# Performance work log

Measured on AMD Instinct MI355X. Metric: run time of the kernel, lower is better.

The kernel has to match this reference:

```python
import jax, jax.numpy as jnp
import numpy as np
import math

B, C, HLAT, WLON = 1, 256, 46, 90
HEADS = 8
KC = 256   # k_channels (defaults to in_channels)
OC = 256   # out_channels (defaults to in_channels)


def _cc_weights(n):
    # Clenshaw-Curtis quadrature weights on n nodes x_k = cos(k*pi/(n-1)) over [-1, 1]
    # (torch-harmonics 'equiangular' grid quadrature); weights sum to 2.
    N = n - 1
    k = np.arange(n)
    j = np.arange(1, N // 2 + 1)
    b = np.where(2 * j == N, 1.0, 2.0)
    s = (b / (4.0 * j**2 - 1.0))[None, :] * np.cos(2.0 * np.pi * np.outer(k, j) / N)
    w = (1.0 - s.sum(axis=1)) * (2.0 / N)
    w[0] *= 0.5
    w[-1] *= 0.5
    return w


def _log_quad_weights(nlat, nlon):
    wgl = _cc_weights(nlat).astype(np.float32)            # [nlat]
    qw = 2.0 * np.pi * wgl / nlon                          # [nlat]
    qw = np.tile(qw.reshape(-1, 1), (1, nlon)).flatten()   # [nlat*nlon]
    return np.log(qw).reshape(1, 1, -1)                    # (1, 1, N)


def setup_inputs() -> dict:
    key = jax.random.key(0)
    ks = jax.random.split(key, 6)
    scale_qkv = math.sqrt(3.0 / C)
    scale_proj = math.sqrt(3.0 / OC)
    uni = lambda k, shp, s: s * (2.0 * jax.random.uniform(k, shp, dtype=jnp.float32) - 1.0)
    return {
        "query": jax.random.normal(ks[0], (B, C, HLAT, WLON), dtype=jnp.float32),
        "q_w": uni(ks[1], (KC, C), scale_qkv),
        "q_b": jnp.zeros((KC,), dtype=jnp.float32),
        "k_w": uni(ks[2], (KC, C), scale_qkv),
        "k_b": jnp.zeros((KC,), dtype=jnp.float32),
        "v_w": uni(ks[3], (OC, C), scale_qkv),
        "v_b": jnp.zeros((OC,), dtype=jnp.float32),
        "p_w": uni(ks[4], (OC, OC), scale_proj),
        "p_b": jnp.zeros((OC,), dtype=jnp.float32),
        "log_qw": jnp.asarray(_log_quad_weights(HLAT, WLON)),
    }


def _conv1x1(x, w, b):
    # 1x1 conv == per-pixel channel GEMM
    return jnp.einsum("bchw,kc->bkhw", x, w) + b[None, :, None, None]


def _to_seq(x, heads):
    # [B, heads*d, H, W] -> [B, heads, H*W, d]
    b, c, h, w = x.shape
    d = c // heads
    return x.reshape(b, heads, d, h, w).transpose(0, 1, 3, 4, 2).reshape(b, heads, h * w, d)


def reference(query, q_w, q_b, k_w, k_b, v_w, v_b, p_w, p_b, log_qw):
    # key = value = query (self-attention path of the module)
    q = _conv1x1(query, q_w, q_b)
    k = _conv1x1(query, k_w, k_b)
    v = _conv1x1(query, v_w, v_b)

    qs = _to_seq(q, HEADS)   # [B, h, N, dk]
    ks = _to_seq(k, HEADS)   # [B, h, M, dk]
    vs = _to_seq(v, HEADS)   # [B, h, M, dv]

    dk = KC // HEADS
    scale = 1.0 / math.sqrt(dk)  # SDPA default scale
    # scores with additive log-quadrature-weight bias over keys
    scores = jnp.einsum("bhnd,bhmd->bhnm", qs, ks) * scale + log_qw[:, :, None, :]
    attn = jax.nn.softmax(scores, axis=-1)
    out = jnp.einsum("bhnm,bhmd->bhnd", attn, vs)  # [B, h, N, dv]

    bb, hh, nn, dv = out.shape
    out = out.transpose(0, 1, 3, 2).reshape(bb, hh * dv, HLAT, WLON)
    out = _conv1x1(out, p_w, p_b)
    return out
```

## Files before the change

### kernel.cpp

```cpp
#include <hip/hip_runtime.h>

#define N_SEQ 4140
#define NP    4160
#define C_IN  256
#define HEADS 8
#define NT32  130
#define HN    (HEADS * N_SEQ)
#define LOG2E 1.4426950408889634f
#define SCALE2 (0.17677669529663687f * LOG2E)
#define INVSCALE 5.656854249492381f

typedef _Float16 f16x8 __attribute__((ext_vector_type(8)));
typedef float    f32x16 __attribute__((ext_vector_type(16)));

__device__ inline unsigned short f16b(float x) {
    union { _Float16 h; unsigned short s; } c;
    c.h = (_Float16)x;
    return c.s;
}
__device__ inline unsigned pack2h(float lo, float hi) {
    union { _Float16 h[2]; unsigned u; } c;
    c.h[0] = (_Float16)lo;
    c.h[1] = (_Float16)hi;
    return c.u;
}
__device__ inline void permswap(unsigned &a, unsigned &b) {
    asm volatile("v_permlane32_swap_b32 %0, %1" : "+v"(a), "+v"(b));
}

__global__ __launch_bounds__(256) void convert_x(
    const float* __restrict__ x, unsigned short* __restrict__ xt)
{
    __shared__ unsigned short tile[32][33];
    const int tx = threadIdx.x & 31, ty = threadIdx.x >> 5;
    const int n0 = blockIdx.x * 32, c0 = blockIdx.y * 32;
#pragma unroll
    for (int i = 0; i < 4; ++i) {
        const int c = c0 + ty * 4 + i;
        const int n = n0 + tx;
        const float v = (n < N_SEQ) ? x[(size_t)c * N_SEQ + n] : 0.f;
        tile[tx][ty * 4 + i] = f16b(v);
    }
    __syncthreads();
#pragma unroll
    for (int i = 0; i < 4; ++i) {
        const int nl = ty * 4 + i;
        xt[(size_t)(n0 + nl) * C_IN + c0 + tx] = tile[nl][tx];
    }
}

__global__ __launch_bounds__(256) void init_misc(
    const float* __restrict__ log_qw,
    const float* __restrict__ q_w, const float* __restrict__ k_w,
    const float* __restrict__ v_w, const float* __restrict__ p_w,
    float* __restrict__ lw2, unsigned short* __restrict__ wf,
    unsigned short* __restrict__ pwf)
{
    const int i = blockIdx.x * 256 + threadIdx.x;
    if (i < NP) lw2[i] = (i < N_SEQ) ? log_qw[i] * INVSCALE : -1e30f;
    if (i < 65536)       wf[i] = f16b(q_w[i]);
    else if (i < 131072) wf[i] = f16b(k_w[i - 65536]);
    else if (i < 196608) wf[i] = f16b(v_w[i - 131072]);
    if (i < 65536) pwf[i] = f16b(p_w[i]);
}

__global__ __launch_bounds__(256) void qkv_mfma(
    const unsigned short* __restrict__ xt, const unsigned short* __restrict__ wf,
    const float* __restrict__ q_b, const float* __restrict__ k_b,
    const float* __restrict__ v_b,
    unsigned short* __restrict__ qo, unsigned short* __restrict__ ko,
    unsigned short* __restrict__ vo)
{
    const int tid = threadIdx.x, wid = tid >> 6, lane = tid & 63;
    const int col = lane & 31, hi = lane >> 5;
    const int tile = blockIdx.x * 4 + wid;
    const int ot = tile / NT32, nt = tile % NT32;
    const int n0 = nt * 32;
    const bool vmode = (ot >= 16);

    const unsigned short* arow;
    const unsigned short* brow;
    if (!vmode) {
        arow = xt + (size_t)(n0 + col) * C_IN + hi * 8;
        brow = wf + (size_t)(ot * 32 + col) * C_IN + hi * 8;
    } else {
        arow = wf + (size_t)(512 + (ot - 16) * 32 + col) * C_IN + hi * 8;
        brow = xt + (size_t)(n0 + col) * C_IN + hi * 8;
    }

    f32x16 acc;
    if (!vmode) {
        const float bias = (ot < 8) ? q_b[ot * 32 + col] : k_b[(ot - 8) * 32 + col];
#pragma unroll
        for (int r = 0; r < 16; ++r) acc[r] = bias;
    } else {
        const float* vb4 = v_b + (ot - 16) * 32 + 4 * hi;
        const float4 b0 = *(const float4*)(vb4);
        const float4 b1 = *(const float4*)(vb4 + 8);
        const float4 b2 = *(const float4*)(vb4 + 16);
        const float4 b3 = *(const float4*)(vb4 + 24);
        acc[0]=b0.x; acc[1]=b0.y; acc[2]=b0.z; acc[3]=b0.w;
        acc[4]=b1.x; acc[5]=b1.y; acc[6]=b1.z; acc[7]=b1.w;
        acc[8]=b2.x; acc[9]=b2.y; acc[10]=b2.z; acc[11]=b2.w;
        acc[12]=b3.x; acc[13]=b3.y; acc[14]=b3.z; acc[15]=b3.w;
    }

#pragma unroll
    for (int t = 0; t < 16; ++t) {
        const f16x8 af = *(const f16x8*)(const void*)(arow + t * 16);
        const f16x8 bf = *(const f16x8*)(const void*)(brow + t * 16);
        acc = __builtin_amdgcn_mfma_f32_32x32x16_f16(af, bf, acc, 0, 0, 0);
    }

    if (!vmode) {
        unsigned short* dst = (ot < 8) ? qo : ko;
        const int h = ot & 7;
#pragma unroll
        for (int r = 0; r < 16; ++r) {
            const int n = n0 + (r & 3) + 8 * (r >> 2) + 4 * hi;
            dst[(size_t)(h * NP + n) * 32 + col] = f16b(acc[r]);
        }
    } else {
        const int h = ot - 16;
#pragma unroll
        for (int r = 0; r < 16; ++r) {
            const int d = (r & 3) + 8 * (r >> 2) + 4 * hi;
            vo[((size_t)(h * NT32 + nt) * 32 + d) * 32 + col] = f16b(acc[r]);
        }
    }
}

__global__ __launch_bounds__(256) void attn_mfma_kernel(
    const unsigned short* __restrict__ qb, const unsigned short* __restrict__ kb,
    const unsigned short* __restrict__ vb, const float* __restrict__ lw2,
    float* __restrict__ pm, float* __restrict__ pl, float* __restrict__ pacc,
    int tiles_per_z)
{
    const int tid = threadIdx.x;
    const int wid = tid >> 6;
    const int lane = tid & 63;
    const int col = lane & 31;
    const int hi = lane >> 5;
    const int job = blockIdx.x * 4 + wid;
    const int h = job / NT32;
    const int qt = job % NT32;
    const int z = blockIdx.y;

    const int qrow = qt * 32 + col;
    const unsigned short* qp = qb + ((size_t)(h * NP + qrow)) * 32 + hi * 8;
    const f16x8 qf0 = *(const f16x8*)(const void*)(qp);
    const f16x8 qf1 = *(const f16x8*)(const void*)(qp + 16);

    f32x16 o;
#pragma unroll
    for (int r = 0; r < 16; ++r) o[r] = 0.f;
    float m = -1e30f, lsum = 0.f;

    const int t0 = z * tiles_per_z;
    const int t1 = min(NT32, t0 + tiles_per_z);
    const unsigned short* kbase = kb + (size_t)h * NP * 32;
    const unsigned short* vbase = vb + (size_t)h * NT32 * 1024;

    for (int t = t0; t < t1; ++t) {
        const int k0 = t * 32;
        const unsigned short* kp = kbase + (size_t)(k0 + col) * 32 + hi * 8;
        const f16x8 ka0 = *(const f16x8*)(const void*)(kp);
        const f16x8 ka1 = *(const f16x8*)(const void*)(kp + 16);
        const unsigned short* vp = vbase + (size_t)t * 1024 + col * 32 + hi * 8;
        const f16x8 va0 = *(const f16x8*)(const void*)(vp);
        const f16x8 va1 = *(const f16x8*)(const void*)(vp + 16);

        const float* lw4 = lw2 + k0 + 4 * hi;
        const float4 w0 = *(const float4*)(lw4);
        const float4 w1 = *(const float4*)(lw4 + 8);
        const float4 w2 = *(const float4*)(lw4 + 16);
        const float4 w3 = *(const float4*)(lw4 + 24);
        f32x16 s;
        s[0]=w0.x; s[1]=w0.y; s[2]=w0.z; s[3]=w0.w;
        s[4]=w1.x; s[5]=w1.y; s[6]=w1.z; s[7]=w1.w;
        s[8]=w2.x; s[9]=w2.y; s[10]=w2.z; s[11]=w2.w;
        s[12]=w3.x; s[13]=w3.y; s[14]=w3.z; s[15]=w3.w;

        s = __builtin_amdgcn_mfma_f32_32x32x16_f16(ka0, qf0, s, 0, 0, 0);
        s = __builtin_amdgcn_mfma_f32_32x32x16_f16(ka1, qf1, s, 0, 0, 0);

        float p[16];
#pragma unroll
        for (int r = 0; r < 16; ++r) p[r] = s[r] * SCALE2;

        float x0 = fmaxf(p[0], p[1]),   x1 = fmaxf(p[2], p[3]);
        float x2 = fmaxf(p[4], p[5]),   x3 = fmaxf(p[6], p[7]);
        float x4 = fmaxf(p[8], p[9]),   x5 = fmaxf(p[10], p[11]);
        float x6 = fmaxf(p[12], p[13]), x7 = fmaxf(p[14], p[15]);
        x0 = fmaxf(x0, x1); x2 = fmaxf(x2, x3);
        x4 = fmaxf(x4, x5); x6 = fmaxf(x6, x7);
        const float cmax = fmaxf(fmaxf(x0, x2), fmaxf(x4, x6));

        if (!__all(cmax - m <= 8.0f)) {
            float cw = fmaxf(cmax, __shfl_xor(cmax, 32));
            const float mnew = fmaxf(m, cw);
            const float esc = __builtin_amdgcn_exp2f(m - mnew);
            lsum *= esc;
#pragma unroll
            for (int r = 0; r < 16; ++r) o[r] *= esc;
            m = mnew;
        }

#pragma unroll
        for (int r = 0; r < 16; ++r) p[r] = __builtin_amdgcn_exp2f(p[r] - m);
        {
            float s0 = (p[0] + p[1]) + (p[2] + p[3]);
            float s1 = (p[4] + p[5]) + (p[6] + p[7]);
            float s2 = (p[8] + p[9]) + (p[10] + p[11]);
            float s3 = (p[12] + p[13]) + (p[14] + p[15]);
            lsum += (s0 + s1) + (s2 + s3);
        }

        union U { unsigned u[4]; f16x8 v; };
        unsigned a0 = pack2h(p[0], p[1]),  b0 = pack2h(p[2], p[3]);
        unsigned c0 = pack2h(p[4], p[5]),  d0 = pack2h(p[6], p[7]);
        permswap(a0, c0);
        permswap(b0, d0);
        U pb0; pb0.u[0] = a0; pb0.u[1] = b0; pb0.u[2] = c0; pb0.u[3] = d0;
        o = __builtin_amdgcn_mfma_f32_32x32x16_f16(va0, pb0.v, o, 0, 0, 0);

        unsigned e0 = pack2h(p[8], p[9]),   f0 = pack2h(p[10], p[11]);
        unsigned g0 = pack2h(p[12], p[13]), h0 = pack2h(p[14], p[15]);
        permswap(e0, g0);
        permswap(f0, h0);
        U pb1; pb1.u[0] = e0; pb1.u[1] = f0; pb1.u[2] = g0; pb1.u[3] = h0;
        o = __builtin_amdgcn_mfma_f32_32x32x16_f16(va1, pb1.v, o, 0, 0, 0);
    }

    lsum += __shfl_xor(lsum, 32);

    if (qrow < N_SEQ) {
        const size_t qi = (size_t)h * N_SEQ + qrow;
        if (hi == 0) {
            pm[(size_t)z * HN + qi] = m;
            pl[(size_t)z * HN + qi] = lsum;
        }
        float* pa = pacc + ((size_t)z * HN + qi) * 32;
#pragma unroll
        for (int r = 0; r < 16; ++r)
            pa[(r & 3) + 8 * (r >> 2) + 4 * hi] = o[r];
    }
}

__global__ __launch_bounds__(256) void merge_kernel(
    const float* __restrict__ pm, const float* __restrict__ pl,
    const float* __restrict__ pacc, unsigned short* __restrict__ at_t, int nz)
{
    const int idx = blockIdx.x * 256 + threadIdx.x;
    if (idx >= HN) return;
    const int h = idx / N_SEQ;
    const int n = idx - h * N_SEQ;

    float mg = pm[idx];
    for (int zz = 1; zz < nz; ++zz) mg = fmaxf(mg, pm[(size_t)zz * HN + idx]);

    float lg = 0.f;
    float acc[32];
#pragma unroll
    for (int d = 0; d < 32; ++d) acc[d] = 0.f;
    for (int zz = 0; zz < nz; ++zz) {
        const float e = exp2f(pm[(size_t)zz * HN + idx] - mg);
        lg += pl[(size_t)zz * HN + idx] * e;
        const float* pa = pacc + ((size_t)zz * HN + idx) * 32;
#pragma unroll
        for (int d = 0; d < 32; ++d) acc[d] = fmaf(pa[d], e, acc[d]);
    }
    const float inv = 1.0f / lg;
    union { unsigned short s[32]; uint4 u[4]; } ph;
#pragma unroll
    for (int d = 0; d < 32; ++d) ph.s[d] = f16b(acc[d] * inv);
    uint4* dst = (uint4*)(at_t + (size_t)n * C_IN + h * 32);
#pragma unroll
    for (int i = 0; i < 4; ++i) dst[i] = ph.u[i];
}

__global__ __launch_bounds__(256) void proj_mfma(
    const unsigned short* __restrict__ at_t, const unsigned short* __restrict__ pwf,
    const float* __restrict__ p_b, float* __restrict__ out)
{
    const int tid = threadIdx.x, wid = tid >> 6, lane = tid & 63;
    const int col = lane & 31, hi = lane >> 5;
    const int tile = blockIdx.x * 4 + wid;
    const int ot = tile / NT32, nt = tile % NT32;
    const int n0 = nt * 32;

    const unsigned short* arow = pwf + (size_t)(ot * 32 + col) * C_IN + hi * 8;
    const unsigned short* brow = at_t + (size_t)(n0 + col) * C_IN + hi * 8;

    const float* pb4 = p_b + ot * 32 + 4 * hi;
    const float4 b0 = *(const float4*)(pb4);
    const float4 b1 = *(const float4*)(pb4 + 8);
    const float4 b2 = *(const float4*)(pb4 + 16);
    const float4 b3 = *(const float4*)(pb4 + 24);
    f32x16 acc;
    acc[0]=b0.x; acc[1]=b0.y; acc[2]=b0.z; acc[3]=b0.w;
    acc[4]=b1.x; acc[5]=b1.y; acc[6]=b1.z; acc[7]=b1.w;
    acc[8]=b2.x; acc[9]=b2.y; acc[10]=b2.z; acc[11]=b2.w;
    acc[12]=b3.x; acc[13]=b3.y; acc[14]=b3.z; acc[15]=b3.w;

#pragma unroll
    for (int t = 0; t < 16; ++t) {
        const f16x8 af = *(const f16x8*)(const void*)(arow + t * 16);
        const f16x8 bf = *(const f16x8*)(const void*)(brow + t * 16);
        acc = __builtin_amdgcn_mfma_f32_32x32x16_f16(af, bf, acc, 0, 0, 0);
    }

    const int n = n0 + col;
    if (n < N_SEQ) {
#pragma unroll
        for (int r = 0; r < 16; ++r) {
            const int oc = ot * 32 + (r & 3) + 8 * (r >> 2) + 4 * hi;
            out[(size_t)oc * N_SEQ + n] = acc[r];
        }
    }
}

extern "C" void kernel_launch(void* const* d_in, const int* in_sizes, int n_in,
                              void* d_out, int out_size, void* d_ws, size_t ws_size,
                              hipStream_t stream) {
    const float* query  = (const float*)d_in[0];
    const float* q_w    = (const float*)d_in[1];
    const float* q_b    = (const float*)d_in[2];
    const float* k_w    = (const float*)d_in[3];
    const float* k_b    = (const float*)d_in[4];
    const float* v_w    = (const float*)d_in[5];
    const float* v_b    = (const float*)d_in[6];
    const float* p_w    = (const float*)d_in[7];
    const float* p_b    = (const float*)d_in[8];
    const float* log_qw = (const float*)d_in[9];

    const size_t HNP32 = (size_t)HEADS * NP * 32;

    unsigned short* xt  = (unsigned short*)d_ws;
    unsigned short* qb  = xt + (size_t)NP * C_IN;
    unsigned short* kb  = qb + HNP32;
    unsigned short* vb  = kb + HNP32;
    unsigned short* wf  = vb + HNP32;
    unsigned short* pwf = wf + 768 * 256;
    float* lw2 = (float*)(pwf + 256 * 256);
    float* pm  = lw2 + NP;
    unsigned short* at_t = qb;

    const size_t base_bytes = (size_t)((char*)pm - (char*)d_ws);
    const size_t per_z = (size_t)HN * 34 * sizeof(float);
    int nz = 1;
    if      (ws_size >= base_bytes + 8 * per_z) nz = 8;
    else if (ws_size >= base_bytes + 4 * per_z) nz = 4;
    else if (ws_size >= base_bytes + 2 * per_z) nz = 2;
    const int tiles_per_z = (NT32 + nz - 1) / nz;

    float* pl   = pm + (size_t)nz * HN;
    float* pacc = pl + (size_t)nz * HN;

    convert_x<<<dim3(NT32, 8), 256, 0, stream>>>(query, xt);

    init_misc<<<dim3(768), 256, 0, stream>>>(
        log_qw, q_w, k_w, v_w, p_w, lw2, wf, pwf);

    qkv_mfma<<<dim3(780), 256, 0, stream>>>(
        xt, wf, q_b, k_b, v_b, qb, kb, vb);

    attn_mfma_kernel<<<dim3(260, nz), 256, 0, stream>>>(
        qb, kb, vb, lw2, pm, pl, pacc, tiles_per_z);

    merge_kernel<<<dim3((HN + 255) / 256), 256, 0, stream>>>(
        pm, pl, pacc, at_t, nz);

    proj_mfma<<<dim3(260), 256, 0, stream>>>(
        at_t, pwf, p_b, (float*)d_out);
}
```

Baseline: 174.7 us.

## Process two query tiles per wave, merge prep kernels, and cap split-K at four

```diff
diff --git a/kernel.cpp b/kernel.cpp
--- a/kernel.cpp
+++ b/kernel.cpp
@@ -28,40 +28,43 @@
     asm volatile("v_permlane32_swap_b32 %0, %1" : "+v"(a), "+v"(b));
 }
 
-__global__ __launch_bounds__(256) void convert_x(
-    const float* __restrict__ x, unsigned short* __restrict__ xt)
-{
-    __shared__ unsigned short tile[32][33];
-    const int tx = threadIdx.x & 31, ty = threadIdx.x >> 5;
-    const int n0 = blockIdx.x * 32, c0 = blockIdx.y * 32;
-#pragma unroll
-    for (int i = 0; i < 4; ++i) {
-        const int c = c0 + ty * 4 + i;
-        const int n = n0 + tx;
-        const float v = (n < N_SEQ) ? x[(size_t)c * N_SEQ + n] : 0.f;
-        tile[tx][ty * 4 + i] = f16b(v);
-    }
-    __syncthreads();
-#pragma unroll
-    for (int i = 0; i < 4; ++i) {
-        const int nl = ty * 4 + i;
-        xt[(size_t)(n0 + nl) * C_IN + c0 + tx] = tile[nl][tx];
-    }
-}
-
-__global__ __launch_bounds__(256) void init_misc(
-    const float* __restrict__ log_qw,
+__global__ __launch_bounds__(256) void prep_kernel(
+    const float* __restrict__ x, const float* __restrict__ log_qw,
     const float* __restrict__ q_w, const float* __restrict__ k_w,
     const float* __restrict__ v_w, const float* __restrict__ p_w,
-    float* __restrict__ lw2, unsigned short* __restrict__ wf,
-    unsigned short* __restrict__ pwf)
+    unsigned short* __restrict__ xt, float* __restrict__ lw2,
+    unsigned short* __restrict__ wf, unsigned short* __restrict__ pwf)
 {
-    const int i = blockIdx.x * 256 + threadIdx.x;
-    if (i < NP) lw2[i] = (i < N_SEQ) ? log_qw[i] * INVSCALE : -1e30f;
-    if (i < 65536)       wf[i] = f16b(q_w[i]);
-    else if (i < 131072) wf[i] = f16b(k_w[i - 65536]);
-    else if (i < 196608) wf[i] = f16b(v_w[i - 131072]);
-    if (i < 65536) pwf[i] = f16b(p_w[i]);
+    if (blockIdx.x < NT32) {
+        __shared__ unsigned short tile[32][33];
+        const int tx = threadIdx.x & 31, ty = threadIdx.x >> 5;
+        const int n0 = blockIdx.x * 32, c0 = blockIdx.y * 32;
+#pragma unroll
+        for (int i = 0; i < 4; ++i) {
+            const int c = c0 + ty * 4 + i;
+            const int n = n0 + tx;
+            const float v = (n < N_SEQ) ? x[(size_t)c * N_SEQ + n] : 0.f;
+            tile[tx][ty * 4 + i] = f16b(v);
+        }
+        __syncthreads();
+#pragma unroll
+        for (int i = 0; i < 4; ++i) {
+            const int nl = ty * 4 + i;
+            xt[(size_t)(n0 + nl) * C_IN + c0 + tx] = tile[nl][tx];
+        }
+    } else {
+        const int bid = (blockIdx.x - NT32) * 8 + blockIdx.y;
+        for (int i = bid * 256 + threadIdx.x; i < 262144 + NP; i += 24 * 256) {
+            if (i < 65536)        wf[i] = f16b(q_w[i]);
+            else if (i < 131072)  wf[i] = f16b(k_w[i - 65536]);
+            else if (i < 196608)  wf[i] = f16b(v_w[i - 131072]);
+            else if (i < 262144)  pwf[i - 196608] = f16b(p_w[i - 196608]);
+            else {
+                const int j = i - 262144;
+                lw2[j] = (j < N_SEQ) ? log_qw[j] * INVSCALE : -1e30f;
+            }
+        }
+    }
 }
 
 __global__ __launch_bounds__(256) void qkv_mfma(
@@ -73,59 +76,64 @@
 {
     const int tid = threadIdx.x, wid = tid >> 6, lane = tid & 63;
     const int col = lane & 31, hi = lane >> 5;
-    const int tile = blockIdx.x * 4 + wid;
-    const int ot = tile / NT32, nt = tile % NT32;
-    const int n0 = nt * 32;
-    const bool vmode = (ot >= 16);
-
-    const unsigned short* arow;
-    const unsigned short* brow;
-    if (!vmode) {
-        arow = xt + (size_t)(n0 + col) * C_IN + hi * 8;
-        brow = wf + (size_t)(ot * 32 + col) * C_IN + hi * 8;
-    } else {
-        arow = wf + (size_t)(512 + (ot - 16) * 32 + col) * C_IN + hi * 8;
-        brow = xt + (size_t)(n0 + col) * C_IN + hi * 8;
-    }
-
-    f32x16 acc;
-    if (!vmode) {
+    const int w = blockIdx.x * 4 + wid;
+    const int ot = w / 65, pt = w % 65;
+    const int n0 = pt * 64, n1 = n0 + 32;
+
+    if (ot < 16) {
+        const unsigned short* a0 = xt + (size_t)(n0 + col) * C_IN + hi * 8;
+        const unsigned short* a1 = xt + (size_t)(n1 + col) * C_IN + hi * 8;
+        const unsigned short* bw = wf + (size_t)(ot * 32 + col) * C_IN + hi * 8;
         const float bias = (ot < 8) ? q_b[ot * 32 + col] : k_b[(ot - 8) * 32 + col];
-#pragma unroll
-        for (int r = 0; r < 16; ++r) acc[r] = bias;
-    } else {
-        const float* vb4 = v_b + (ot - 16) * 32 + 4 * hi;
-        const float4 b0 = *(const float4*)(vb4);
-        const float4 b1 = *(const float4*)(vb4 + 8);
-        const float4 b2 = *(const float4*)(vb4 + 16);
-        const float4 b3 = *(const float4*)(vb4 + 24);
-        acc[0]=b0.x; acc[1]=b0.y; acc[2]=b0.z; acc[3]=b0.w;
-        acc[4]=b1.x; acc[5]=b1.y; acc[6]=b1.z; acc[7]=b1.w;
-        acc[8]=b2.x; acc[9]=b2.y; acc[10]=b2.z; acc[11]=b2.w;
-        acc[12]=b3.x; acc[13]=b3.y; acc[14]=b3.z; acc[15]=b3.w;
-    }
-
-#pragma unroll
-    for (int t = 0; t < 16; ++t) {
-        const f16x8 af = *(const f16x8*)(const void*)(arow + t * 16);
-        const f16x8 bf = *(const f16x8*)(const void*)(brow + t * 16);
-        acc = __builtin_amdgcn_mfma_f32_32x32x16_f16(af, bf, acc, 0, 0, 0);
-    }
-
-    if (!vmode) {
+        f32x16 acc0, acc1;
+#pragma unroll
+        for (int r = 0; r < 16; ++r) { acc0[r] = bias; acc1[r] = bias; }
+#pragma unroll
+        for (int t = 0; t < 16; ++t) {
+            const f16x8 bf  = *(const f16x8*)(const void*)(bw + t * 16);
+            const f16x8 af0 = *(const f16x8*)(const void*)(a0 + t * 16);
+            const f16x8 af1 = *(const f16x8*)(const void*)(a1 + t * 16);
+            acc0 = __builtin_amdgcn_mfma_f32_32x32x16_f16(af0, bf, acc0, 0, 0, 0);
+            acc1 = __builtin_amdgcn_mfma_f32_32x32x16_f16(af1, bf, acc1, 0, 0, 0);
+        }
         unsigned short* dst = (ot < 8) ? qo : ko;
         const int h = ot & 7;
 #pragma unroll
         for (int r = 0; r < 16; ++r) {
-            const int n = n0 + (r & 3) + 8 * (r >> 2) + 4 * hi;
-            dst[(size_t)(h * NP + n) * 32 + col] = f16b(acc[r]);
+            const int rl = (r & 3) + 8 * (r >> 2) + 4 * hi;
+            dst[(size_t)(h * NP + n0 + rl) * 32 + col] = f16b(acc0[r]);
+            dst[(size_t)(h * NP + n1 + rl) * 32 + col] = f16b(acc1[r]);
         }
     } else {
         const int h = ot - 16;
+        const unsigned short* aw = wf + (size_t)(512 + h * 32 + col) * C_IN + hi * 8;
+        const unsigned short* b0 = xt + (size_t)(n0 + col) * C_IN + hi * 8;
+        const unsigned short* b1 = xt + (size_t)(n1 + col) * C_IN + hi * 8;
+        const float* vb4 = v_b + h * 32 + 4 * hi;
+        const float4 c0 = *(const float4*)(vb4);
+        const float4 c1 = *(const float4*)(vb4 + 8);
+        const float4 c2 = *(const float4*)(vb4 + 16);
+        const float4 c3 = *(const float4*)(vb4 + 24);
+        f32x16 acc0;
+        acc0[0]=c0.x; acc0[1]=c0.y; acc0[2]=c0.z; acc0[3]=c0.w;
+        acc0[4]=c1.x; acc0[5]=c1.y; acc0[6]=c1.z; acc0[7]=c1.w;
+        acc0[8]=c2.x; acc0[9]=c2.y; acc0[10]=c2.z; acc0[11]=c2.w;
+        acc0[12]=c3.x; acc0[13]=c3.y; acc0[14]=c3.z; acc0[15]=c3.w;
+        f32x16 acc1 = acc0;
+#pragma unroll
+        for (int t = 0; t < 16; ++t) {
+            const f16x8 af  = *(const f16x8*)(const void*)(aw + t * 16);
+            const f16x8 bf0 = *(const f16x8*)(const void*)(b0 + t * 16);
+            const f16x8 bf1 = *(const f16x8*)(const void*)(b1 + t * 16);
+            acc0 = __builtin_amdgcn_mfma_f32_32x32x16_f16(af, bf0, acc0, 0, 0, 0);
+            acc1 = __builtin_amdgcn_mfma_f32_32x32x16_f16(af, bf1, acc1, 0, 0, 0);
+        }
+        const int nt0 = pt * 2, nt1 = nt0 + 1;
 #pragma unroll
         for (int r = 0; r < 16; ++r) {
             const int d = (r & 3) + 8 * (r >> 2) + 4 * hi;
-            vo[((size_t)(h * NT32 + nt) * 32 + d) * 32 + col] = f16b(acc[r]);
+            vo[((size_t)(h * NT32 + nt0) * 32 + d) * 32 + col] = f16b(acc0[r]);
+            vo[((size_t)(h * NT32 + nt1) * 32 + d) * 32 + col] = f16b(acc1[r]);
         }
     }
 }
@@ -142,19 +150,24 @@
     const int col = lane & 31;
     const int hi = lane >> 5;
     const int job = blockIdx.x * 4 + wid;
-    const int h = job / NT32;
-    const int qt = job % NT32;
+    const int h = job / 65;
+    const int pt = job % 65;
     const int z = blockIdx.y;
 
-    const int qrow = qt * 32 + col;
-    const unsigned short* qp = qb + ((size_t)(h * NP + qrow)) * 32 + hi * 8;
-    const f16x8 qf0 = *(const f16x8*)(const void*)(qp);
-    const f16x8 qf1 = *(const f16x8*)(const void*)(qp + 16);
-
-    f32x16 o;
-#pragma unroll
-    for (int r = 0; r < 16; ++r) o[r] = 0.f;
-    float m = -1e30f, lsum = 0.f;
+    const int qrowA = pt * 64 + col;
+    const int qrowB = qrowA + 32;
+    const unsigned short* qpA = qb + ((size_t)(h * NP + qrowA)) * 32 + hi * 8;
+    const unsigned short* qpB = qb + ((size_t)(h * NP + qrowB)) * 32 + hi * 8;
+    const f16x8 qfA0 = *(const f16x8*)(const void*)(qpA);
+    const f16x8 qfA1 = *(const f16x8*)(const void*)(qpA + 16);
+    const f16x8 qfB0 = *(const f16x8*)(const void*)(qpB);
+    const f16x8 qfB1 = *(const f16x8*)(const void*)(qpB + 16);
+
+    f32x16 oA, oB;
+#pragma unroll
+    for (int r = 0; r < 16; ++r) { oA[r] = 0.f; oB[r] = 0.f; }
+    float mA = -1e30f, lsA = 0.f;
+    float mB = -1e30f, lsB = 0.f;
 
     const int t0 = z * tiles_per_z;
     const int t1 = min(NT32, t0 + tiles_per_z);
@@ -175,75 +188,125 @@
         const float4 w1 = *(const float4*)(lw4 + 8);
         const float4 w2 = *(const float4*)(lw4 + 16);
         const float4 w3 = *(const float4*)(lw4 + 24);
-        f32x16 s;
-        s[0]=w0.x; s[1]=w0.y; s[2]=w0.z; s[3]=w0.w;
-        s[4]=w1.x; s[5]=w1.y; s[6]=w1.z; s[7]=w1.w;
-        s[8]=w2.x; s[9]=w2.y; s[10]=w2.z; s[11]=w2.w;
-        s[12]=w3.x; s[13]=w3.y; s[14]=w3.z; s[15]=w3.w;
-
-        s = __builtin_amdgcn_mfma_f32_32x32x16_f16(ka0, qf0, s, 0, 0, 0);
-        s = __builtin_amdgcn_mfma_f32_32x32x16_f16(ka1, qf1, s, 0, 0, 0);
-
-        float p[16];
-#pragma unroll
-        for (int r = 0; r < 16; ++r) p[r] = s[r] * SCALE2;
-
-        float x0 = fmaxf(p[0], p[1]),   x1 = fmaxf(p[2], p[3]);
-        float x2 = fmaxf(p[4], p[5]),   x3 = fmaxf(p[6], p[7]);
-        float x4 = fmaxf(p[8], p[9]),   x5 = fmaxf(p[10], p[11]);
-        float x6 = fmaxf(p[12], p[13]), x7 = fmaxf(p[14], p[15]);
-        x0 = fmaxf(x0, x1); x2 = fmaxf(x2, x3);
-        x4 = fmaxf(x4, x5); x6 = fmaxf(x6, x7);
-        const float cmax = fmaxf(fmaxf(x0, x2), fmaxf(x4, x6));
-
-        if (!__all(cmax - m <= 8.0f)) {
-            float cw = fmaxf(cmax, __shfl_xor(cmax, 32));
-            const float mnew = fmaxf(m, cw);
-            const float esc = __builtin_amdgcn_exp2f(m - mnew);
-            lsum *= esc;
-#pragma unroll
-            for (int r = 0; r < 16; ++r) o[r] *= esc;
-            m = mnew;
-        }
-
-#pragma unroll
-        for (int r = 0; r < 16; ++r) p[r] = __builtin_amdgcn_exp2f(p[r] - m);
+        f32x16 sI;
+        sI[0]=w0.x; sI[1]=w0.y; sI[2]=w0.z; sI[3]=w0.w;
+        sI[4]=w1.x; sI[5]=w1.y; sI[6]=w1.z; sI[7]=w1.w;
+        sI[8]=w2.x; sI[9]=w2.y; sI[10]=w2.z; sI[11]=w2.w;
+        sI[12]=w3.x; sI[13]=w3.y; sI[14]=w3.z; sI[15]=w3.w;
+
+        f32x16 sA = sI, sB = sI;
+        sA = __builtin_amdgcn_mfma_f32_32x32x16_f16(ka0, qfA0, sA, 0, 0, 0);
+        sB = __builtin_amdgcn_mfma_f32_32x32x16_f16(ka0, qfB0, sB, 0, 0, 0);
+        sA = __builtin_amdgcn_mfma_f32_32x32x16_f16(ka1, qfA1, sA, 0, 0, 0);
+        sB = __builtin_amdgcn_mfma_f32_32x32x16_f16(ka1, qfB1, sB, 0, 0, 0);
+
+        float pA[16], pB[16];
+#pragma unroll
+        for (int r = 0; r < 16; ++r) { pA[r] = sA[r] * SCALE2; pB[r] = sB[r] * SCALE2; }
+
+        float ax0 = fmaxf(pA[0], pA[1]),   ax1 = fmaxf(pA[2], pA[3]);
+        float ax2 = fmaxf(pA[4], pA[5]),   ax3 = fmaxf(pA[6], pA[7]);
+        float ax4 = fmaxf(pA[8], pA[9]),   ax5 = fmaxf(pA[10], pA[11]);
+        float ax6 = fmaxf(pA[12], pA[13]), ax7 = fmaxf(pA[14], pA[15]);
+        float bx0 = fmaxf(pB[0], pB[1]),   bx1 = fmaxf(pB[2], pB[3]);
+        float bx2 = fmaxf(pB[4], pB[5]),   bx3 = fmaxf(pB[6], pB[7]);
+        float bx4 = fmaxf(pB[8], pB[9]),   bx5 = fmaxf(pB[10], pB[11]);
+        float bx6 = fmaxf(pB[12], pB[13]), bx7 = fmaxf(pB[14], pB[15]);
+        ax0 = fmaxf(ax0, ax1); ax2 = fmaxf(ax2, ax3);
+        ax4 = fmaxf(ax4, ax5); ax6 = fmaxf(ax6, ax7);
+        bx0 = fmaxf(bx0, bx1); bx2 = fmaxf(bx2, bx3);
+        bx4 = fmaxf(bx4, bx5); bx6 = fmaxf(bx6, bx7);
+        const float cmaxA = fmaxf(fmaxf(ax0, ax2), fmaxf(ax4, ax6));
+        const float cmaxB = fmaxf(fmaxf(bx0, bx2), fmaxf(bx4, bx6));
+
+        if (!__all(cmaxA - mA <= 8.0f)) {
+            float cw = fmaxf(cmaxA, __shfl_xor(cmaxA, 32));
+            const float mnew = fmaxf(mA, cw);
+            const float esc = __builtin_amdgcn_exp2f(mA - mnew);
+            lsA *= esc;
+#pragma unroll
+            for (int r = 0; r < 16; ++r) oA[r] *= esc;
+            mA = mnew;
+        }
+        if (!__all(cmaxB - mB <= 8.0f)) {
+            float cw = fmaxf(cmaxB, __shfl_xor(cmaxB, 32));
+            const float mnew = fmaxf(mB, cw);
+            const float esc = __builtin_amdgcn_exp2f(mB - mnew);
+            lsB *= esc;
+#pragma unroll
+            for (int r = 0; r < 16; ++r) oB[r] *= esc;
+            mB = mnew;
+        }
+
+#pragma unroll
+        for (int r = 0; r < 16; ++r) {
+            pA[r] = __builtin_amdgcn_exp2f(pA[r] - mA);
+            pB[r] = __builtin_amdgcn_exp2f(pB[r] - mB);
+        }
         {
-            float s0 = (p[0] + p[1]) + (p[2] + p[3]);
-            float s1 = (p[4] + p[5]) + (p[6] + p[7]);
-            float s2 = (p[8] + p[9]) + (p[10] + p[11]);
-            float s3 = (p[12] + p[13]) + (p[14] + p[15]);
-            lsum += (s0 + s1) + (s2 + s3);
+            float s0 = (pA[0] + pA[1]) + (pA[2] + pA[3]);
+            float s1 = (pA[4] + pA[5]) + (pA[6] + pA[7]);
+            float s2 = (pA[8] + pA[9]) + (pA[10] + pA[11]);
+            float s3 = (pA[12] + pA[13]) + (pA[14] + pA[15]);
+            lsA += (s0 + s1) + (s2 + s3);
+            float u0 = (pB[0] + pB[1]) + (pB[2] + pB[3]);
+            float u1 = (pB[4] + pB[5]) + (pB[6] + pB[7]);
+            float u2 = (pB[8] + pB[9]) + (pB[10] + pB[11]);
+            float u3 = (pB[12] + pB[13]) + (pB[14] + pB[15]);
+            lsB += (u0 + u1) + (u2 + u3);
         }
 
         union U { unsigned u[4]; f16x8 v; };
-        unsigned a0 = pack2h(p[0], p[1]),  b0 = pack2h(p[2], p[3]);
-        unsigned c0 = pack2h(p[4], p[5]),  d0 = pack2h(p[6], p[7]);
-        permswap(a0, c0);
-        permswap(b0, d0);
-        U pb0; pb0.u[0] = a0; pb0.u[1] = b0; pb0.u[2] = c0; pb0.u[3] = d0;
-        o = __builtin_amdgcn_mfma_f32_32x32x16_f16(va0, pb0.v, o, 0, 0, 0);
-
-        unsigned e0 = pack2h(p[8], p[9]),   f0 = pack2h(p[10], p[11]);
-        unsigned g0 = pack2h(p[12], p[13]), h0 = pack2h(p[14], p[15]);
-        permswap(e0, g0);
-        permswap(f0, h0);
-        U pb1; pb1.u[0] = e0; pb1.u[1] = f0; pb1.u[2] = g0; pb1.u[3] = h0;
-        o = __builtin_amdgcn_mfma_f32_32x32x16_f16(va1, pb1.v, o, 0, 0, 0);
-    }
-
-    lsum += __shfl_xor(lsum, 32);
-
-    if (qrow < N_SEQ) {
-        const size_t qi = (size_t)h * N_SEQ + qrow;
+        {
+            unsigned a0 = pack2h(pA[0], pA[1]),  b0 = pack2h(pA[2], pA[3]);
+            unsigned c0 = pack2h(pA[4], pA[5]),  d0 = pack2h(pA[6], pA[7]);
+            permswap(a0, c0); permswap(b0, d0);
+            U pb0; pb0.u[0]=a0; pb0.u[1]=b0; pb0.u[2]=c0; pb0.u[3]=d0;
+            oA = __builtin_amdgcn_mfma_f32_32x32x16_f16(va0, pb0.v, oA, 0, 0, 0);
+            unsigned e0 = pack2h(pA[8], pA[9]),   f0 = pack2h(pA[10], pA[11]);
+            unsigned g0 = pack2h(pA[12], pA[13]), h0 = pack2h(pA[14], pA[15]);
+            permswap(e0, g0); permswap(f0, h0);
+            U pb1; pb1.u[0]=e0; pb1.u[1]=f0; pb1.u[2]=g0; pb1.u[3]=h0;
+            oA = __builtin_amdgcn_mfma_f32_32x32x16_f16(va1, pb1.v, oA, 0, 0, 0);
+        }
+        {
+            unsigned a0 = pack2h(pB[0], pB[1]),  b0 = pack2h(pB[2], pB[3]);
+            unsigned c0 = pack2h(pB[4], pB[5]),  d0 = pack2h(pB[6], pB[7]);
+            permswap(a0, c0); permswap(b0, d0);
+            U pb0; pb0.u[0]=a0; pb0.u[1]=b0; pb0.u[2]=c0; pb0.u[3]=d0;
+            oB = __builtin_amdgcn_mfma_f32_32x32x16_f16(va0, pb0.v, oB, 0, 0, 0);
+            unsigned e0 = pack2h(pB[8], pB[9]),   f0 = pack2h(pB[10], pB[11]);
+            unsigned g0 = pack2h(pB[12], pB[13]), h0 = pack2h(pB[14], pB[15]);
+            permswap(e0, g0); permswap(f0, h0);
+            U pb1; pb1.u[0]=e0; pb1.u[1]=f0; pb1.u[2]=g0; pb1.u[3]=h0;
+            oB = __builtin_amdgcn_mfma_f32_32x32x16_f16(va1, pb1.v, oB, 0, 0, 0);
+        }
+    }
+
+    lsA += __shfl_xor(lsA, 32);
+    lsB += __shfl_xor(lsB, 32);
+
+    if (qrowA < N_SEQ) {
+        const size_t qi = (size_t)h * N_SEQ + qrowA;
         if (hi == 0) {
-            pm[(size_t)z * HN + qi] = m;
-            pl[(size_t)z * HN + qi] = lsum;
+            pm[(size_t)z * HN + qi] = mA;
+            pl[(size_t)z * HN + qi] = lsA;
         }
         float* pa = pacc + ((size_t)z * HN + qi) * 32;
 #pragma unroll
         for (int r = 0; r < 16; ++r)
-            pa[(r & 3) + 8 * (r >> 2) + 4 * hi] = o[r];
+            pa[(r & 3) + 8 * (r >> 2) + 4 * hi] = oA[r];
+    }
+    if (qrowB < N_SEQ) {
+        const size_t qi = (size_t)h * N_SEQ + qrowB;
+        if (hi == 0) {
+            pm[(size_t)z * HN + qi] = mB;
+            pl[(size_t)z * HN + qi] = lsB;
+        }
+        float* pa = pacc + ((size_t)z * HN + qi) * 32;
+#pragma unroll
+        for (int r = 0; r < 16; ++r)
+            pa[(r & 3) + 8 * (r >> 2) + 4 * hi] = oB[r];
     }
 }
 
@@ -293,21 +356,26 @@
     const unsigned short* brow = at_t + (size_t)(n0 + col) * C_IN + hi * 8;
 
     const float* pb4 = p_b + ot * 32 + 4 * hi;
-    const float4 b0 = *(const float4*)(pb4);
-    const float4 b1 = *(const float4*)(pb4 + 8);
-    const float4 b2 = *(const float4*)(pb4 + 16);
-    const float4 b3 = *(const float4*)(pb4 + 24);
-    f32x16 acc;
-    acc[0]=b0.x; acc[1]=b0.y; acc[2]=b0.z; acc[3]=b0.w;
-    acc[4]=b1.x; acc[5]=b1.y; acc[6]=b1.z; acc[7]=b1.w;
-    acc[8]=b2.x; acc[9]=b2.y; acc[10]=b2.z; acc[11]=b2.w;
-    acc[12]=b3.x; acc[13]=b3.y; acc[14]=b3.z; acc[15]=b3.w;
-
-#pragma unroll
-    for (int t = 0; t < 16; ++t) {
-        const f16x8 af = *(const f16x8*)(const void*)(arow + t * 16);
-        const f16x8 bf = *(const f16x8*)(const void*)(brow + t * 16);
-        acc = __builtin_amdgcn_mfma_f32_32x32x16_f16(af, bf, acc, 0, 0, 0);
+    const float4 c0 = *(const float4*)(pb4);
+    const float4 c1 = *(const float4*)(pb4 + 8);
+    const float4 c2 = *(const float4*)(pb4 + 16);
+    const float4 c3 = *(const float4*)(pb4 + 24);
+    f32x16 acca, accb;
+    acca[0]=c0.x; acca[1]=c0.y; acca[2]=c0.z; acca[3]=c0.w;
+    acca[4]=c1.x; acca[5]=c1.y; acca[6]=c1.z; acca[7]=c1.w;
+    acca[8]=c2.x; acca[9]=c2.y; acca[10]=c2.z; acca[11]=c2.w;
+    acca[12]=c3.x; acca[13]=c3.y; acca[14]=c3.z; acca[15]=c3.w;
+#pragma unroll
+    for (int r = 0; r < 16; ++r) accb[r] = 0.f;
+
+#pragma unroll
+    for (int t = 0; t < 8; ++t) {
+        const f16x8 afa = *(const f16x8*)(const void*)(arow + t * 16);
+        const f16x8 bfa = *(const f16x8*)(const void*)(brow + t * 16);
+        const f16x8 afb = *(const f16x8*)(const void*)(arow + (t + 8) * 16);
+        const f16x8 bfb = *(const f16x8*)(const void*)(brow + (t + 8) * 16);
+        acca = __builtin_amdgcn_mfma_f32_32x32x16_f16(afa, bfa, acca, 0, 0, 0);
+        accb = __builtin_amdgcn_mfma_f32_32x32x16_f16(afb, bfb, accb, 0, 0, 0);
     }
 
     const int n = n0 + col;
@@ -315,7 +383,7 @@
 #pragma unroll
         for (int r = 0; r < 16; ++r) {
             const int oc = ot * 32 + (r & 3) + 8 * (r >> 2) + 4 * hi;
-            out[(size_t)oc * N_SEQ + n] = acc[r];
+            out[(size_t)oc * N_SEQ + n] = acca[r] + accb[r];
         }
     }
 }
@@ -349,23 +417,20 @@
     const size_t base_bytes = (size_t)((char*)pm - (char*)d_ws);
     const size_t per_z = (size_t)HN * 34 * sizeof(float);
     int nz = 1;
-    if      (ws_size >= base_bytes + 8 * per_z) nz = 8;
-    else if (ws_size >= base_bytes + 4 * per_z) nz = 4;
+    if      (ws_size >= base_bytes + 4 * per_z) nz = 4;
     else if (ws_size >= base_bytes + 2 * per_z) nz = 2;
     const int tiles_per_z = (NT32 + nz - 1) / nz;
 
     float* pl   = pm + (size_t)nz * HN;
     float* pacc = pl + (size_t)nz * HN;
 
-    convert_x<<<dim3(NT32, 8), 256, 0, stream>>>(query, xt);
-
-    init_misc<<<dim3(768), 256, 0, stream>>>(
-        log_qw, q_w, k_w, v_w, p_w, lw2, wf, pwf);
-
-    qkv_mfma<<<dim3(780), 256, 0, stream>>>(
+    prep_kernel<<<dim3(NT32 + 3, 8), 256, 0, stream>>>(
+        query, log_qw, q_w, k_w, v_w, p_w, xt, lw2, wf, pwf);
+
+    qkv_mfma<<<dim3(390), 256, 0, stream>>>(
         xt, wf, q_b, k_b, v_b, qb, kb, vb);
 
-    attn_mfma_kernel<<<dim3(260, nz), 256, 0, stream>>>(
+    attn_mfma_kernel<<<dim3(130, nz), 256, 0, stream>>>(
         qb, kb, vb, lw2, pm, pl, pacc, tiles_per_z);
 
     merge_kernel<<<dim3((HN + 255) / 256), 256, 0, stream>>>(
```

Result: slower. 181.0 us (+3.6%).
